# Kernel optimization log

Measured on AMD Instinct MI355X. Metric: run time of the kernel, lower is better.

Reference implementation:

```python
import jax, jax.numpy as jnp
import numpy as np

B, LQ, LK = 4, 512, 512
QS, KS, H, DV = 512, 512, 256, 512


def setup_inputs() -> dict:
    key = jax.random.key(0)
    ks = jax.random.split(key, 9)
    s_q = 1.0 / np.sqrt(QS)
    s_k = 1.0 / np.sqrt(KS)
    s_v = 1.0 / np.sqrt(H)
    return {
        "query": jax.random.normal(ks[0], (B, LQ, QS), jnp.float32),
        "key": jax.random.normal(ks[1], (B, LK, KS), jnp.float32),
        "value": jax.random.normal(ks[2], (B, LK, DV), jnp.float32),
        "wq": jax.random.uniform(ks[3], (H, QS), jnp.float32, -s_q, s_q),
        "bq": jax.random.uniform(ks[4], (H,), jnp.float32, -s_q, s_q),
        "wk": jax.random.uniform(ks[5], (H, KS), jnp.float32, -s_k, s_k),
        "bk": jax.random.uniform(ks[6], (H,), jnp.float32, -s_k, s_k),
        "wv": jax.random.uniform(ks[7], (H,), jnp.float32, -s_v, s_v),
        "bv": jax.random.uniform(ks[8], (), jnp.float32, -s_v, s_v),
    }


def reference(query, key, value, wq, bq, wk, bk, wv, bv):
    # q: [B, Lq, H], k: [B, Lk, H]
    q = jnp.einsum('bqd,hd->bqh', query, wq) + bq
    k = jnp.einsum('bkd,hd->bkh', key, wk) + bk
    # broadcast add -> [B, Lq, Lk, H], tanh, project to scalar score
    feats = jnp.tanh(q[:, :, None, :] + k[:, None, :, :])
    scores = jnp.einsum('bqkh,h->bqk', feats, wv) + bv  # [B, Lq, Lk]
    attn = jax.nn.softmax(scores, axis=-1)
    # dropout p=0.0 (identity at inference)
    return jnp.einsum('bqk,bkd->bqd', attn, value)
```

## Files before the change

### kernel.cpp

```cpp
#include <hip/hip_runtime.h>

#define LOG2E 1.4426950408889634f

constexpr int Bb = 4, LQ = 512, LK = 512, QS = 512, H = 256, DV = 512;
constexpr int M = 2048;

constexpr size_t OFF_EQT = 0;
constexpr size_t OFF_EKT = 2u << 20;
constexpr size_t OFF_PQ  = 4u << 20;
constexpr size_t OFF_ROW = 6u << 20;
constexpr size_t OFF_VT  = 8u << 20;

using bf16x8 = __attribute__((ext_vector_type(8))) short;
using f32x4v = __attribute__((ext_vector_type(4))) float;

__device__ inline unsigned short f2bf(float x) {
    unsigned int u = __float_as_uint(x);
    u += 0x7FFFu + ((u >> 16) & 1u);
    return (unsigned short)(u >> 16);
}
__device__ inline unsigned int pk2(float lo, float hi) {
    unsigned int r;
    asm("v_cvt_pk_bf16_f32 %0, %1, %2" : "=v"(r) : "v"(lo), "v"(hi));
    return r;
}

__global__ __launch_bounds__(256) void proj_mfma(
    const float* __restrict__ query, const float* __restrict__ key,
    const float* __restrict__ wq, const float* __restrict__ wk,
    const float* __restrict__ bq, const float* __restrict__ bk,
    char* __restrict__ ws, float scale)
{
    const int z = blockIdx.z;
    const float* A    = z ? key : query;
    const float* W    = z ? wk : wq;
    const float* bias = z ? bk : bq;
    float* out = (float*)(ws + (z ? OFF_EKT : OFF_EQT));

    __shared__ unsigned short Als[64][136];
    __shared__ unsigned short Wls[64][136];
    __shared__ float Ot[64][68];

    const int mb = blockIdx.x * 64, nb = blockIdx.y * 64;
    const int tid = threadIdx.x;
    const int wid = tid >> 6, lane = tid & 63;
    const int ml = lane & 15, quad = lane >> 4;

    f32x4v acc[4] = {{0,0,0,0},{0,0,0,0},{0,0,0,0},{0,0,0,0}};

    for (int kc = 0; kc < QS; kc += 128) {
        __syncthreads();
#pragma unroll
        for (int it = 0; it < 4; ++it) {
            int u = tid + it * 256;
            int row = u >> 4, c8 = (u & 15) * 8;
            float4 a0 = *(const float4*)(A + (size_t)(mb + row) * 512 + kc + c8);
            float4 a1 = *(const float4*)(A + (size_t)(mb + row) * 512 + kc + c8 + 4);
            uint4 pa = { pk2(a0.x, a0.y), pk2(a0.z, a0.w), pk2(a1.x, a1.y), pk2(a1.z, a1.w) };
            *(uint4*)&Als[row][c8] = pa;
            float4 w0 = *(const float4*)(W + (size_t)(nb + row) * 512 + kc + c8);
            float4 w1 = *(const float4*)(W + (size_t)(nb + row) * 512 + kc + c8 + 4);
            uint4 pw = { pk2(w0.x, w0.y), pk2(w0.z, w0.w), pk2(w1.x, w1.y), pk2(w1.z, w1.w) };
            *(uint4*)&Wls[row][c8] = pw;
        }
        __syncthreads();
#pragma unroll
        for (int s = 0; s < 4; ++s) {
            int k = s * 32 + quad * 8;
            bf16x8 af = *(const bf16x8*)&Als[wid * 16 + ml][k];
#pragma unroll
            for (int nt = 0; nt < 4; ++nt) {
                bf16x8 bfr = *(const bf16x8*)&Wls[nt * 16 + ml][k];
                acc[nt] = __builtin_amdgcn_mfma_f32_16x16x32_bf16(af, bfr, acc[nt], 0, 0, 0);
            }
        }
    }
    __syncthreads();
#pragma unroll
    for (int nt = 0; nt < 4; ++nt)
#pragma unroll
        for (int r = 0; r < 4; ++r)
            Ot[nt * 16 + ml][wid * 16 + quad * 4 + r] = acc[nt][r];
    __syncthreads();
    {
        int r0 = tid >> 2;
        int c0 = (tid & 3) * 16;
        float bs = bias[nb + r0];
#pragma unroll
        for (int g = 0; g < 4; ++g) {
            float4 v = *(const float4*)&Ot[r0][c0 + g * 4];
            float4 o;
            o.x = __builtin_amdgcn_exp2f(fminf(fmaxf(scale * (v.x + bs), -15.f), 15.f));
            o.y = __builtin_amdgcn_exp2f(fminf(fmaxf(scale * (v.y + bs), -15.f), 15.f));
            o.z = __builtin_amdgcn_exp2f(fminf(fmaxf(scale * (v.z + bs), -15.f), 15.f));
            o.w = __builtin_amdgcn_exp2f(fminf(fmaxf(scale * (v.w + bs), -15.f), 15.f));
            *(float4*)(out + (size_t)(nb + r0) * 2048 + mb + c0 + g * 4) = o;
        }
    }
}

__global__ __launch_bounds__(256) void vconv(
    const float* __restrict__ V, char* __restrict__ ws)
{
    unsigned short* VT = (unsigned short*)(ws + OFF_VT);
    __shared__ unsigned short T[64][72];
    const int b = blockIdx.z, k0 = blockIdx.x * 64, n0 = blockIdx.y * 64;
    const int tid = threadIdx.x;
    const float* Vb = V + (size_t)b * 512 * 512;
    const int r = tid >> 4, c = (tid & 15) * 4;
#pragma unroll
    for (int it = 0; it < 4; ++it) {
        int kr = r + it * 16;
        float4 v = *(const float4*)(Vb + (size_t)(k0 + kr) * 512 + n0 + c);
        T[c + 0][kr] = f2bf(v.x);
        T[c + 1][kr] = f2bf(v.y);
        T[c + 2][kr] = f2bf(v.z);
        T[c + 3][kr] = f2bf(v.w);
    }
    __syncthreads();
    const int rowO = tid >> 3, colO = (tid & 7) * 8;
#pragma unroll
    for (int it = 0; it < 2; ++it) {
        int n = rowO + it * 32;
        uint4 o = *(const uint4*)&T[n][colO];
        *(uint4*)(VT + ((size_t)b * 512 + n0 + n) * 512 + k0 + colO) = o;
    }
}

__global__ __launch_bounds__(512, 2) void score_kernel(
    const float* __restrict__ wvp, char* __restrict__ ws)
{
    const float* EqT = (const float*)(ws + OFF_EQT);
    const float* EkT = (const float*)(ws + OFF_EKT);
    unsigned short* Pq = (unsigned short*)(ws + OFF_PQ);
    float* rowpart = (float*)(ws + OFF_ROW);

    __shared__ float Qs[64][64];
    __shared__ float Ks[64][64];
    __shared__ float Wv2[H];
    __shared__ float redS[8][64];

    const int b  = blockIdx.z;
    const int qb = blockIdx.x * 64;
    const int kt = blockIdx.y;
    const int kb = kt * 64;
    const int tid = threadIdx.x;
    const int tx = tid & 15;
    const int ty = tid >> 4;
    const int w  = tid >> 6;
    const int lane = tid & 63;

    if (tid < H) Wv2[tid] = wvp[tid] * (2.0f * LOG2E);

    const int mq = b * LQ + qb;
    const int mk = b * LK + kb;
    const int sh = tid >> 4;
    const int sm = (tid & 15) * 4;

    float acc[4][2] = {};

    for (int h0 = 0; h0 < H; h0 += 64) {
        __syncthreads();
#pragma unroll
        for (int it = 0; it < 2; ++it) {
            int h = sh + 32 * it;
            *(float4*)&Qs[h][sm] = *(const float4*)(EqT + (size_t)(h0 + h) * M + mq + sm);
            *(float4*)&Ks[h][sm] = *(const float4*)(EkT + (size_t)(h0 + h) * M + mk + sm);
        }
        __syncthreads();
#pragma unroll 4
        for (int hh = 0; hh < 64; hh += 4) {
            float4 q1 = *(const float4*)&Qs[hh][tx * 4];
            float4 q2 = *(const float4*)&Qs[hh + 1][tx * 4];
            float4 q3 = *(const float4*)&Qs[hh + 2][tx * 4];
            float4 q4 = *(const float4*)&Qs[hh + 3][tx * 4];
            float2 k1 = *(const float2*)&Ks[hh][ty * 2];
            float2 k2 = *(const float2*)&Ks[hh + 1][ty * 2];
            float2 k3 = *(const float2*)&Ks[hh + 2][ty * 2];
            float2 k4 = *(const float2*)&Ks[hh + 3][ty * 2];
            float4 w4v = *(const float4*)&Wv2[h0 + hh];
            const float w1 = w4v.x, w2 = w4v.y, w3 = w4v.z, w4 = w4v.w;
            const float q1a[4] = {q1.x, q1.y, q1.z, q1.w};
            const float q2a[4] = {q2.x, q2.y, q2.z, q2.w};
            const float q3a[4] = {q3.x, q3.y, q3.z, q3.w};
            const float q4a[4] = {q4.x, q4.y, q4.z, q4.w};
            const float k1a[2] = {k1.x, k1.y};
            const float k2a[2] = {k2.x, k2.y};
            const float k3a[2] = {k3.x, k3.y};
            const float k4a[2] = {k4.x, k4.y};
#pragma unroll
            for (int i = 0; i < 4; ++i)
#pragma unroll
                for (int j = 0; j < 2; ++j) {
                    float ta = fmaf(q1a[i], k1a[j], 1.0f);
                    float tb = fmaf(q2a[i], k2a[j], 1.0f);
                    float tc = fmaf(q3a[i], k3a[j], 1.0f);
                    float td = fmaf(q4a[i], k4a[j], 1.0f);
                    float t12 = ta * tb;
                    float t34 = tc * td;
                    float n12 = fmaf(w1, tb, w2 * ta);
                    float n34 = fmaf(w3, td, w4 * tc);
                    float num = fmaf(n12, t34, n34 * t12);
                    float den = t12 * t34;
                    acc[i][j] = fmaf(num, __builtin_amdgcn_rcpf(den), acc[i][j]);
                }
        }
    }

    float ps[4];
#pragma unroll
    for (int i = 0; i < 4; ++i) {
        int q = qb + tx * 4 + i;
        float p0 = __builtin_amdgcn_exp2f(-acc[i][0]);
        float p1 = __builtin_amdgcn_exp2f(-acc[i][1]);
        ps[i] = p0 + p1;
        *(unsigned int*)(Pq + ((size_t)(b * 512 + q) * 512 + kb + ty * 2)) = pk2(p0, p1);
    }
#pragma unroll
    for (int i = 0; i < 4; ++i) {
        ps[i] += __shfl_xor(ps[i], 16, 64);
        ps[i] += __shfl_xor(ps[i], 32, 64);
    }
    if (lane < 16) {
#pragma unroll
        for (int i = 0; i < 4; ++i) redS[w][tx * 4 + i] = ps[i];
    }
    __syncthreads();
    if (tid < 64) {
        float s = ((redS[0][tid] + redS[1][tid]) + (redS[2][tid] + redS[3][tid]))
                + ((redS[4][tid] + redS[5][tid]) + (redS[6][tid] + redS[7][tid]));
        rowpart[(size_t)kt * 2048 + b * 512 + qb + tid] = s;
    }
}

__global__ __launch_bounds__(512, 2) void av_mfma(
    const char* __restrict__ wsc, float* __restrict__ O)
{
    const unsigned short* Pq = (const unsigned short*)(wsc + OFF_PQ);
    const unsigned short* VT = (const unsigned short*)(wsc + OFF_VT);
    const float* rowpart = (const float*)(wsc + OFF_ROW);

    __shared__ unsigned short Pls[64][136];
    __shared__ unsigned short Vls[64][136];

    const int b = blockIdx.z, qb = blockIdx.x * 64, nb = blockIdx.y * 64;
    const int tid = threadIdx.x;
    const int wid = tid >> 6, lane = tid & 63;
    const int ml = lane & 15, quad = lane >> 4;
    const int ms = wid & 3, nh = wid >> 2;
    const unsigned short* Pb = Pq + (size_t)b * 512 * 512;
    const unsigned short* Vb = VT + (size_t)b * 512 * 512;

    f32x4v acc[2] = {{0,0,0,0},{0,0,0,0}};

    for (int kc = 0; kc < LK; kc += 128) {
        __syncthreads();
#pragma unroll
        for (int it = 0; it < 2; ++it) {
            int u = tid + it * 512;
            int row = u >> 4, c8 = (u & 15) * 8;
            *(uint4*)&Pls[row][c8] = *(const uint4*)(Pb + (size_t)(qb + row) * 512 + kc + c8);
            *(uint4*)&Vls[row][c8] = *(const uint4*)(Vb + (size_t)(nb + row) * 512 + kc + c8);
        }
        __syncthreads();
#pragma unroll
        for (int s = 0; s < 4; ++s) {
            int k = s * 32 + quad * 8;
            bf16x8 af = *(const bf16x8*)&Pls[ms * 16 + ml][k];
#pragma unroll
            for (int t = 0; t < 2; ++t) {
                bf16x8 bfr = *(const bf16x8*)&Vls[(nh * 2 + t) * 16 + ml][k];
                acc[t] = __builtin_amdgcn_mfma_f32_16x16x32_bf16(af, bfr, acc[t], 0, 0, 0);
            }
        }
    }

    float rr[4];
#pragma unroll
    for (int r = 0; r < 4; ++r) {
        int q = qb + ms * 16 + quad * 4 + r;
        float rs = 0.f;
#pragma unroll
        for (int t8 = 0; t8 < 8; ++t8) rs += rowpart[(size_t)t8 * 2048 + b * 512 + q];
        rr[r] = 1.0f / rs;
    }
#pragma unroll
    for (int t = 0; t < 2; ++t)
#pragma unroll
        for (int r = 0; r < 4; ++r) {
            int q = qb + ms * 16 + quad * 4 + r;
            O[((size_t)b * 512 + q) * 512 + nb + (nh * 2 + t) * 16 + ml] = acc[t][r] * rr[r];
        }
}

extern "C" void kernel_launch(void* const* d_in, const int* in_sizes, int n_in,
                              void* d_out, int out_size, void* d_ws, size_t ws_size,
                              hipStream_t stream) {
    const float* query = (const float*)d_in[0];
    const float* key   = (const float*)d_in[1];
    const float* value = (const float*)d_in[2];
    const float* wq    = (const float*)d_in[3];
    const float* bq    = (const float*)d_in[4];
    const float* wk    = (const float*)d_in[5];
    const float* bk    = (const float*)d_in[6];
    const float* wv    = (const float*)d_in[7];
    float* out = (float*)d_out;
    char* ws = (char*)d_ws;

    const float c2 = 2.0f * LOG2E;

    proj_mfma<<<dim3(32, 4, 2), 256, 0, stream>>>(query, key, wq, wk, bq, bk, ws, c2);
    vconv<<<dim3(8, 8, Bb), 256, 0, stream>>>(value, ws);
    score_kernel<<<dim3(8, 8, Bb), 512, 0, stream>>>(wv, ws);
    av_mfma<<<dim3(8, 8, Bb), 512, 0, stream>>>(ws, out);
}
```

Before: 118.9 us.

## Batch tanh products over 8 heads per reciprocal and halve score query tile

The score kernel now combines eight head terms into a single rational sum per reciprocal instead of four. This halves the rcp count per head. To keep the 8-way products within float range, Eq is pre-scaled by 2^-13 in the projection epilogue, the clamp is tightened to ±13, and the additive constant becomes 2^-13 with Wv rescaled to match. The query tile shrinks from 64 to 32 rows per block, which doubles the grid and raises the occupancy hint to 4 blocks. The costs are a larger grid, extra K tile reloads, and some risk of precision loss from the scaled products and narrower clamp.

```diff
diff --git a/kernel.cpp b/kernel.cpp
--- a/kernel.cpp
+++ b/kernel.cpp
@@ -36,6 +36,7 @@
     const float* W    = z ? wk : wq;
     const float* bias = z ? bk : bq;
     float* out = (float*)(ws + (z ? OFF_EKT : OFF_EQT));
+    const float off = z ? 0.0f : 13.0f;
 
     __shared__ unsigned short Als[64][136];
     __shared__ unsigned short Wls[64][136];
@@ -90,10 +91,10 @@
         for (int g = 0; g < 4; ++g) {
             float4 v = *(const float4*)&Ot[r0][c0 + g * 4];
             float4 o;
-            o.x = __builtin_amdgcn_exp2f(fminf(fmaxf(scale * (v.x + bs), -15.f), 15.f));
-            o.y = __builtin_amdgcn_exp2f(fminf(fmaxf(scale * (v.y + bs), -15.f), 15.f));
-            o.z = __builtin_amdgcn_exp2f(fminf(fmaxf(scale * (v.z + bs), -15.f), 15.f));
-            o.w = __builtin_amdgcn_exp2f(fminf(fmaxf(scale * (v.w + bs), -15.f), 15.f));
+            o.x = __builtin_amdgcn_exp2f(fminf(fmaxf(scale * (v.x + bs), -13.f), 13.f) - off);
+            o.y = __builtin_amdgcn_exp2f(fminf(fmaxf(scale * (v.y + bs), -13.f), 13.f) - off);
+            o.z = __builtin_amdgcn_exp2f(fminf(fmaxf(scale * (v.z + bs), -13.f), 13.f) - off);
+            o.w = __builtin_amdgcn_exp2f(fminf(fmaxf(scale * (v.w + bs), -13.f), 13.f) - off);
             *(float4*)(out + (size_t)(nb + r0) * 2048 + mb + c0 + g * 4) = o;
         }
     }
@@ -127,7 +128,7 @@
     }
 }
 
-__global__ __launch_bounds__(512, 2) void score_kernel(
+__global__ __launch_bounds__(512, 4) void score_kernel(
     const float* __restrict__ wvp, char* __restrict__ ws)
 {
     const float* EqT = (const float*)(ws + OFF_EQT);
@@ -135,13 +136,13 @@
     unsigned short* Pq = (unsigned short*)(ws + OFF_PQ);
     float* rowpart = (float*)(ws + OFF_ROW);
 
-    __shared__ float Qs[64][64];
+    __shared__ float Qs[64][32];
     __shared__ float Ks[64][64];
     __shared__ float Wv2[H];
-    __shared__ float redS[8][64];
+    __shared__ float redS[8][32];
 
     const int b  = blockIdx.z;
-    const int qb = blockIdx.x * 64;
+    const int qb = blockIdx.x * 32;
     const int kt = blockIdx.y;
     const int kb = kt * 64;
     const int tid = threadIdx.x;
@@ -150,83 +151,78 @@
     const int w  = tid >> 6;
     const int lane = tid & 63;
 
-    if (tid < H) Wv2[tid] = wvp[tid] * (2.0f * LOG2E);
+    constexpr float S = 0.0001220703125f;
+    if (tid < H) Wv2[tid] = wvp[tid] * (2.0f * LOG2E) * S;
 
     const int mq = b * LQ + qb;
     const int mk = b * LK + kb;
-    const int sh = tid >> 4;
-    const int sm = (tid & 15) * 4;
-
-    float acc[4][2] = {};
+
+    float acc[2][2] = {};
 
     for (int h0 = 0; h0 < H; h0 += 64) {
         __syncthreads();
-#pragma unroll
-        for (int it = 0; it < 2; ++it) {
-            int h = sh + 32 * it;
-            *(float4*)&Qs[h][sm] = *(const float4*)(EqT + (size_t)(h0 + h) * M + mq + sm);
-            *(float4*)&Ks[h][sm] = *(const float4*)(EkT + (size_t)(h0 + h) * M + mk + sm);
-        }
-        __syncthreads();
-#pragma unroll 4
-        for (int hh = 0; hh < 64; hh += 4) {
-            float4 q1 = *(const float4*)&Qs[hh][tx * 4];
-            float4 q2 = *(const float4*)&Qs[hh + 1][tx * 4];
-            float4 q3 = *(const float4*)&Qs[hh + 2][tx * 4];
-            float4 q4 = *(const float4*)&Qs[hh + 3][tx * 4];
-            float2 k1 = *(const float2*)&Ks[hh][ty * 2];
-            float2 k2 = *(const float2*)&Ks[hh + 1][ty * 2];
-            float2 k3 = *(const float2*)&Ks[hh + 2][ty * 2];
-            float2 k4 = *(const float2*)&Ks[hh + 3][ty * 2];
-            float4 w4v = *(const float4*)&Wv2[h0 + hh];
-            const float w1 = w4v.x, w2 = w4v.y, w3 = w4v.z, w4 = w4v.w;
-            const float q1a[4] = {q1.x, q1.y, q1.z, q1.w};
-            const float q2a[4] = {q2.x, q2.y, q2.z, q2.w};
-            const float q3a[4] = {q3.x, q3.y, q3.z, q3.w};
-            const float q4a[4] = {q4.x, q4.y, q4.z, q4.w};
-            const float k1a[2] = {k1.x, k1.y};
-            const float k2a[2] = {k2.x, k2.y};
-            const float k3a[2] = {k3.x, k3.y};
-            const float k4a[2] = {k4.x, k4.y};
-#pragma unroll
-            for (int i = 0; i < 4; ++i)
+        {
+            int hq = tid >> 3, cq = (tid & 7) * 4;
+            *(float4*)&Qs[hq][cq] = *(const float4*)(EqT + (size_t)(h0 + hq) * M + mq + cq);
+            int hk = tid >> 4, ck = (tid & 15) * 4;
+            *(float4*)&Ks[hk][ck]      = *(const float4*)(EkT + (size_t)(h0 + hk) * M + mk + ck);
+            *(float4*)&Ks[hk + 32][ck] = *(const float4*)(EkT + (size_t)(h0 + hk + 32) * M + mk + ck);
+        }
+        __syncthreads();
+#pragma unroll 2
+        for (int hh = 0; hh < 64; hh += 8) {
+            float2 qv[8], kv[8];
+#pragma unroll
+            for (int u = 0; u < 8; ++u) qv[u] = *(const float2*)&Qs[hh + u][tx * 2];
+#pragma unroll
+            for (int u = 0; u < 8; ++u) kv[u] = *(const float2*)&Ks[hh + u][ty * 2];
+            const float4 wA = *(const float4*)&Wv2[h0 + hh];
+            const float4 wB = *(const float4*)&Wv2[h0 + hh + 4];
+#pragma unroll
+            for (int i = 0; i < 2; ++i)
 #pragma unroll
                 for (int j = 0; j < 2; ++j) {
-                    float ta = fmaf(q1a[i], k1a[j], 1.0f);
-                    float tb = fmaf(q2a[i], k2a[j], 1.0f);
-                    float tc = fmaf(q3a[i], k3a[j], 1.0f);
-                    float td = fmaf(q4a[i], k4a[j], 1.0f);
-                    float t12 = ta * tb;
-                    float t34 = tc * td;
-                    float n12 = fmaf(w1, tb, w2 * ta);
-                    float n34 = fmaf(w3, td, w4 * tc);
-                    float num = fmaf(n12, t34, n34 * t12);
-                    float den = t12 * t34;
-                    acc[i][j] = fmaf(num, __builtin_amdgcn_rcpf(den), acc[i][j]);
+                    float t[8];
+#pragma unroll
+                    for (int u = 0; u < 8; ++u)
+                        t[u] = fmaf(i ? qv[u].y : qv[u].x, j ? kv[u].y : kv[u].x, S);
+                    float t12 = t[0] * t[1], t34 = t[2] * t[3];
+                    float n12 = fmaf(wA.x, t[1], wA.y * t[0]);
+                    float n34 = fmaf(wA.z, t[3], wA.w * t[2]);
+                    float numA = fmaf(n12, t34, n34 * t12);
+                    float denA = t12 * t34;
+                    float t56 = t[4] * t[5], t78 = t[6] * t[7];
+                    float m12 = fmaf(wB.x, t[5], wB.y * t[4]);
+                    float m34 = fmaf(wB.z, t[7], wB.w * t[6]);
+                    float numB = fmaf(m12, t78, m34 * t56);
+                    float denB = t56 * t78;
+                    float NUMv = fmaf(numA, denB, numB * denA);
+                    float DENv = denA * denB;
+                    acc[i][j] = fmaf(NUMv, __builtin_amdgcn_rcpf(DENv), acc[i][j]);
                 }
         }
     }
 
-    float ps[4];
-#pragma unroll
-    for (int i = 0; i < 4; ++i) {
-        int q = qb + tx * 4 + i;
+    float ps[2];
+#pragma unroll
+    for (int i = 0; i < 2; ++i) {
+        int q = qb + tx * 2 + i;
         float p0 = __builtin_amdgcn_exp2f(-acc[i][0]);
         float p1 = __builtin_amdgcn_exp2f(-acc[i][1]);
         ps[i] = p0 + p1;
         *(unsigned int*)(Pq + ((size_t)(b * 512 + q) * 512 + kb + ty * 2)) = pk2(p0, p1);
     }
 #pragma unroll
-    for (int i = 0; i < 4; ++i) {
+    for (int i = 0; i < 2; ++i) {
         ps[i] += __shfl_xor(ps[i], 16, 64);
         ps[i] += __shfl_xor(ps[i], 32, 64);
     }
     if (lane < 16) {
 #pragma unroll
-        for (int i = 0; i < 4; ++i) redS[w][tx * 4 + i] = ps[i];
+        for (int i = 0; i < 2; ++i) redS[w][tx * 2 + i] = ps[i];
     }
     __syncthreads();
-    if (tid < 64) {
+    if (tid < 32) {
         float s = ((redS[0][tid] + redS[1][tid]) + (redS[2][tid] + redS[3][tid]))
                 + ((redS[4][tid] + redS[5][tid]) + (redS[6][tid] + redS[7][tid]));
         rowpart[(size_t)kt * 2048 + b * 512 + qb + tid] = s;
@@ -311,6 +307,6 @@
 
     proj_mfma<<<dim3(32, 4, 2), 256, 0, stream>>>(query, key, wq, wk, bq, bk, ws, c2);
     vconv<<<dim3(8, 8, Bb), 256, 0, stream>>>(value, ws);
-    score_kernel<<<dim3(8, 8, Bb), 512, 0, stream>>>(wv, ws);
+    score_kernel<<<dim3(16, 8, Bb), 512, 0, stream>>>(wv, ws);
     av_mfma<<<dim3(8, 8, Bb), 512, 0, stream>>>(ws, out);
 }
```

Measured after the change: 118.7 us. Within noise of the previous version (-0.2%).
